# Kernel tuning notes

Hardware: AMD Instinct MI355X
Metric: run time of the kernel (lower is better)

The kernel has to match this reference:

```python
import jax, jax.numpy as jnp
import numpy as np

BETA = 1.0 / np.sqrt(768.0).astype(np.float32)


def setup_inputs() -> dict:
    key = jax.random.key(0)
    k1, k2, k3 = jax.random.split(key, 3)
    x = jax.random.normal(k1, (32, 512, 768), dtype=jnp.float32)
    # torch nn.Linear(dim, n_prototype).weight has shape [n_prototype, dim]
    w_lookup = jax.random.normal(k2, (4096, 768), dtype=jnp.float32) * 0.02
    # torch nn.Linear(n_prototype, dim).weight has shape [dim, n_prototype]
    w_content = jax.random.normal(k3, (768, 4096), dtype=jnp.float32) * 0.02
    return {"x": x, "w_lookup": w_lookup, "w_content": w_content}


def reference(x, w_lookup, w_content):
    # scores: [b, s, n_prototype] = x @ w_lookup^T, scaled by 1/sqrt(dim)
    scores = jnp.einsum("bsd,pd->bsp", x, w_lookup) * jnp.asarray(BETA, x.dtype)
    lookup = jax.nn.softmax(scores, axis=-1)
    # content: [b, s, dim] = lookup @ w_content^T
    content = jnp.einsum("bsp,dp->bsd", lookup, w_content)
    return content  # dropout is identity in eval / p=0.0
```

## Files before the change

### kernel.cpp

```cpp
#include <hip/hip_runtime.h>
#include <hip/hip_bf16.h>


#define NTOK   16384
#define DIM    768
#define NPROT  4096
#define BETA_F 0.03608439182428583f

typedef __bf16 bf16_t;
typedef __bf16 bf16x8 __attribute__((ext_vector_type(8)));
typedef float  floatx4 __attribute__((ext_vector_type(4)));

__device__ __forceinline__ void async_copy16(const bf16_t* g, void* l) {
  __builtin_amdgcn_global_load_lds(
      (__attribute__((address_space(1))) const void*)g,
      (__attribute__((address_space(3))) void*)l, 16, 0, 0);
}

__global__ __launch_bounds__(256) void cvt_all(
    const float* __restrict__ x, const float* __restrict__ wl,
    const float* __restrict__ wc, bf16_t* __restrict__ xb,
    bf16_t* __restrict__ wlb, bf16_t* __restrict__ wcb,
    int nx8, int nw8, int nc8) {
  int i = blockIdx.x * 256 + threadIdx.x;
  const float* in; bf16_t* out; int k;
  if (i < nx8)            { in = x;  out = xb;  k = i; }
  else if (i < nx8 + nw8) { in = wl; out = wlb; k = i - nx8; }
  else if (i < nx8 + nw8 + nc8) { in = wc; out = wcb; k = i - nx8 - nw8; }
  else return;
  const float4* in4 = (const float4*)in;
  float4 a = in4[2 * k], b = in4[2 * k + 1];
  bf16x8 o;
  o[0] = (bf16_t)a.x; o[1] = (bf16_t)a.y; o[2] = (bf16_t)a.z; o[3] = (bf16_t)a.w;
  o[4] = (bf16_t)b.x; o[5] = (bf16_t)b.y; o[6] = (bf16_t)b.z; o[7] = (bf16_t)b.w;
  ((bf16x8*)out)[k] = o;
}

template <int EPI>
__global__ __launch_bounds__(512, 2)
void gemm256(const bf16_t* __restrict__ A, const bf16_t* __restrict__ B,
             void* __restrict__ Cv, float* __restrict__ rowsum,
             const int K, const int N, const int nN) {
  __shared__ char lds[131072];

  const int tid = threadIdx.x;
  const int l   = tid & 63;
  const int w   = tid >> 6;
  const int wr  = w >> 2;
  const int wc  = w & 3;
  const int lr  = l & 15;
  const int lk  = (l >> 4) << 3;

  const int nwg   = gridDim.x;
  const int chunk = nwg >> 3;
  const int wg    = (blockIdx.x & 7) * chunk + (blockIdx.x >> 3);
  const int m0    = (wg / nN) * 256;
  const int n0    = (wg % nN) * 256;

  int aoff[2][2], boff[2][2];
#pragma unroll
  for (int h = 0; h < 2; ++h)
#pragma unroll
    for (int j = 0; j < 2; ++j) {
      const int s     = j * 8 + w;
      const int mfrag = h * 8 + (s >> 1);
      const int ks    = s & 1;
      aoff[h][j] = (m0 + mfrag * 16 + lr) * K + ks * 32 + lk;
      boff[h][j] = (n0 + mfrag * 16 + lr) * K + ks * 32 + lk;
    }

  auto stageA = [&](int slot, int kt, int h) {
#pragma unroll
    for (int j = 0; j < 2; ++j) {
      const int s  = j * 8 + w;
      const int sf = (h * 8 + (s >> 1)) * 2 + (s & 1);
      async_copy16(A + aoff[h][j] + kt * 64, lds + slot * 65536 + sf * 1024);
    }
  };
  auto stageB = [&](int slot, int kt, int h) {
#pragma unroll
    for (int j = 0; j < 2; ++j) {
      const int s  = j * 8 + w;
      const int sf = (h * 8 + (s >> 1)) * 2 + (s & 1);
      async_copy16(B + boff[h][j] + kt * 64,
                   lds + slot * 65536 + 32768 + sf * 1024);
    }
  };

  bf16x8 af[4][2], bg[4][2];
  auto loadA = [&](int slot, int mh) {
#pragma unroll
    for (int q = 0; q < 4; ++q)
#pragma unroll
      for (int ks = 0; ks < 2; ++ks)
        af[q][ks] = *(const bf16x8*)(lds + slot * 65536 +
                        ((mh * 8 + q * 2 + wr) * 2 + ks) * 1024 + l * 16);
  };
  auto loadB = [&](int slot, int nh, int qb) {
#pragma unroll
    for (int q = 0; q < 2; ++q)
#pragma unroll
      for (int ks = 0; ks < 2; ++ks)
        bg[qb + q][ks] = *(const bf16x8*)(lds + slot * 65536 + 32768 +
                        ((nh * 8 + q * 4 + wc) * 2 + ks) * 1024 + l * 16);
  };

  const floatx4 z = {0.f, 0.f, 0.f, 0.f};
  floatx4 acc[8][4];
#pragma unroll
  for (int mt = 0; mt < 8; ++mt)
#pragma unroll
    for (int nt = 0; nt < 4; ++nt) acc[mt][nt] = z;

  auto mma = [&](int mq, int nq) {
    __builtin_amdgcn_s_setprio(1);
#pragma unroll
    for (int q = 0; q < 4; ++q)
#pragma unroll
      for (int r = 0; r < 2; ++r)
#pragma unroll
        for (int ks = 0; ks < 2; ++ks)
          acc[mq * 4 + q][nq * 2 + r] = __builtin_amdgcn_mfma_f32_16x16x32_bf16(
              af[q][ks], bg[nq * 2 + r][ks], acc[mq * 4 + q][nq * 2 + r], 0, 0, 0);
    __builtin_amdgcn_s_setprio(0);
  };

#define BAR()   __builtin_amdgcn_s_barrier()
#define LGKM0() asm volatile("s_waitcnt lgkmcnt(0)" ::: "memory")
#define VM(n)   asm volatile("s_waitcnt vmcnt(" #n ")" ::: "memory")

  const int T = K >> 6;

  stageA(0, 0, 0); stageB(0, 0, 0); stageB(0, 0, 1); stageA(0, 0, 1);
  stageA(1, 1, 0); stageB(1, 1, 0); stageB(1, 1, 1);
  VM(6);
  BAR();

#pragma unroll 1
  for (int t = 0; t < T - 2; t += 2) {
    loadA(0, 0); loadB(0, 0, 0);
    stageA(1, t + 1, 1);
    BAR(); LGKM0(); mma(0, 0); BAR();
    loadB(0, 1, 2);
    stageA(0, t + 2, 0);
    BAR(); LGKM0(); mma(0, 1); BAR();
    loadA(0, 1);
    stageB(0, t + 2, 0);
    BAR(); LGKM0(); mma(1, 1); BAR();
    stageB(0, t + 2, 1);
    BAR(); mma(1, 0); VM(6); BAR();
    loadA(1, 0); loadB(1, 0, 0);
    stageA(0, t + 2, 1);
    BAR(); LGKM0(); mma(0, 0); BAR();
    loadB(1, 1, 2);
    stageA(1, t + 3, 0);
    BAR(); LGKM0(); mma(0, 1); BAR();
    loadA(1, 1);
    stageB(1, t + 3, 0);
    BAR(); LGKM0(); mma(1, 1); BAR();
    stageB(1, t + 3, 1);
    BAR(); mma(1, 0); VM(6); BAR();
  }

  loadA(0, 0); loadB(0, 0, 0);
  stageA(1, T - 1, 1);
  BAR(); LGKM0(); mma(0, 0); BAR();
  loadB(0, 1, 2);
  BAR(); LGKM0(); mma(0, 1); BAR();
  loadA(0, 1);
  BAR(); LGKM0(); mma(1, 1); BAR();
  BAR(); mma(1, 0); VM(0); BAR();
  loadA(1, 0); loadB(1, 0, 0);
  BAR(); LGKM0(); mma(0, 0); BAR();
  loadB(1, 1, 2);
  BAR(); LGKM0(); mma(0, 1); BAR();
  loadA(1, 1);
  BAR(); LGKM0(); mma(1, 1); BAR();
  mma(1, 0);

#undef BAR
#undef LGKM0
#undef VM

  const int hi4 = (l >> 4) << 2;
  if (EPI == 0) {
    bf16_t* P = (bf16_t*)Cv;
#pragma unroll
    for (int mt = 0; mt < 8; ++mt) {
      const int row = m0 + (mt * 2 + wr) * 16 + hi4;
      float rs[4] = {0.f, 0.f, 0.f, 0.f};
#pragma unroll
      for (int nt = 0; nt < 4; ++nt) {
        const int col = n0 + (nt * 4 + wc) * 16 + lr;
#pragma unroll
        for (int i = 0; i < 4; ++i) {
          const float e = __expf(acc[mt][nt][i] * BETA_F);
          P[(row + i) * N + col] = (bf16_t)e;
          rs[i] += e;
        }
      }
#pragma unroll
      for (int i = 0; i < 4; ++i) {
        float s = rs[i];
        s += __shfl_xor(s, 1);
        s += __shfl_xor(s, 2);
        s += __shfl_xor(s, 4);
        s += __shfl_xor(s, 8);
        if (lr == 0) atomicAdd(&rowsum[row + i], s);
      }
    }
  } else {
    float* O = (float*)Cv;
#pragma unroll
    for (int mt = 0; mt < 8; ++mt) {
      const int row = m0 + (mt * 2 + wr) * 16 + hi4;
#pragma unroll
      for (int i = 0; i < 4; ++i) {
        const float inv = 1.0f / rowsum[row + i];
#pragma unroll
        for (int nt = 0; nt < 4; ++nt)
          O[(row + i) * N + n0 + (nt * 4 + wc) * 16 + lr] = acc[mt][nt][i] * inv;
      }
    }
  }
}

__global__ __launch_bounds__(256) void hopfield_fallback(
    const float* __restrict__ x, const float* __restrict__ wl,
    const float* __restrict__ wc, float* __restrict__ out) {
  __shared__ float  xs[8 * 768];
  __shared__ bf16_t ps[8 * 4096];
  __shared__ float  rs[8];
  const int tid = threadIdx.x;
  const int r0  = blockIdx.x * 8;
  if (tid < 8) rs[tid] = 0.f;
  for (int i = tid; i < 8 * 768; i += 256)
    xs[i] = x[(r0 + (i / 768)) * 768 + (i % 768)];
  __syncthreads();

  float lsum[8] = {0, 0, 0, 0, 0, 0, 0, 0};
  for (int p = tid; p < 4096; p += 256) {
    float s[8] = {0, 0, 0, 0, 0, 0, 0, 0};
    for (int d = 0; d < 768; ++d) {
      const float wv = wl[p * 768 + d];
#pragma unroll
      for (int r = 0; r < 8; ++r) s[r] += xs[r * 768 + d] * wv;
    }
#pragma unroll
    for (int r = 0; r < 8; ++r) {
      const float e = __expf(s[r] * BETA_F);
      ps[r * 4096 + p] = (bf16_t)e;
      lsum[r] += e;
    }
  }
#pragma unroll
  for (int r = 0; r < 8; ++r) atomicAdd(&rs[r], lsum[r]);
  __syncthreads();

  for (int d = tid; d < 768; d += 256) {
    float o[8] = {0, 0, 0, 0, 0, 0, 0, 0};
    for (int p = 0; p < 4096; ++p) {
      const float wv = wc[d * 4096 + p];
#pragma unroll
      for (int r = 0; r < 8; ++r) o[r] += (float)ps[r * 4096 + p] * wv;
    }
#pragma unroll
    for (int r = 0; r < 8; ++r) out[(r0 + r) * 768 + d] = o[r] / rs[r];
  }
}

extern "C" void kernel_launch(void* const* d_in, const int* in_sizes, int n_in,
                              void* d_out, int out_size, void* d_ws, size_t ws_size,
                              hipStream_t stream) {
  (void)in_sizes; (void)n_in; (void)out_size;
  const float* x  = (const float*)d_in[0];
  const float* wl = (const float*)d_in[1];
  const float* wc = (const float*)d_in[2];
  float* out = (float*)d_out;

  const size_t xb_e = (size_t)NTOK * DIM;
  const size_t wl_e = (size_t)NPROT * DIM;
  const size_t wc_e = (size_t)DIM * NPROT;
  const size_t P_e  = (size_t)NTOK * NPROT;
  const size_t need = (xb_e + wl_e + wc_e + P_e) * 2 + (size_t)NTOK * 4;

  if (ws_size >= need) {
    char* ws = (char*)d_ws;
    bf16_t* xb  = (bf16_t*)ws;  ws += xb_e * 2;
    bf16_t* wlb = (bf16_t*)ws;  ws += wl_e * 2;
    bf16_t* wcb = (bf16_t*)ws;  ws += wc_e * 2;
    bf16_t* P   = (bf16_t*)ws;  ws += P_e * 2;
    float* rowsum = (float*)ws;

    hipMemsetAsync(rowsum, 0, NTOK * sizeof(float), stream);
    const int nx8 = (int)(xb_e / 8), nw8 = (int)(wl_e / 8), nc8 = (int)(wc_e / 8);
    cvt_all<<<(nx8 + nw8 + nc8 + 255) / 256, 256, 0, stream>>>(
        x, wl, wc, xb, wlb, wcb, nx8, nw8, nc8);
    gemm256<0><<<dim3((NTOK / 256) * (NPROT / 256)), 512, 0, stream>>>(
        xb, wlb, (void*)P, rowsum, DIM, NPROT, NPROT / 256);
    gemm256<1><<<dim3((NTOK / 256) * (DIM / 256)), 512, 0, stream>>>(
        P, wcb, (void*)out, rowsum, NPROT, DIM, DIM / 256);
  } else {
    hopfield_fallback<<<NTOK / 8, 256, 0, stream>>>(x, wl, wc, out);
  }
}
```

Before: 431.3 us.

## Double-buffer LDS fragments in registers to overlap reads with MFMA in GEMM loop

```diff
diff --git a/kernel.cpp b/kernel.cpp
--- a/kernel.cpp
+++ b/kernel.cpp
@@ -87,22 +87,24 @@
     }
   };
 
-  bf16x8 af[4][2], bg[4][2];
-  auto loadA = [&](int slot, int mh) {
-#pragma unroll
-    for (int q = 0; q < 4; ++q)
+  bf16x8 afA[2][2], afB[2][2];
+  bf16x8 bgA[4][2], bgB[4][2];
+
+  auto loadAf = [&](bf16x8 (&dst)[2][2], int slot, int mq) {
+#pragma unroll
+    for (int q = 0; q < 2; ++q)
 #pragma unroll
       for (int ks = 0; ks < 2; ++ks)
-        af[q][ks] = *(const bf16x8*)(lds + slot * 65536 +
-                        ((mh * 8 + q * 2 + wr) * 2 + ks) * 1024 + l * 16);
-  };
-  auto loadB = [&](int slot, int nh, int qb) {
-#pragma unroll
-    for (int q = 0; q < 2; ++q)
+        dst[q][ks] = *(const bf16x8*)(lds + slot * 65536 +
+                        ((4 * mq + 2 * q + wr) * 2 + ks) * 1024 + l * 16);
+  };
+  auto loadBg = [&](bf16x8 (&dst)[4][2], int slot) {
+#pragma unroll
+    for (int nt = 0; nt < 4; ++nt)
 #pragma unroll
       for (int ks = 0; ks < 2; ++ks)
-        bg[qb + q][ks] = *(const bf16x8*)(lds + slot * 65536 + 32768 +
-                        ((nh * 8 + q * 4 + wc) * 2 + ks) * 1024 + l * 16);
+        dst[nt][ks] = *(const bf16x8*)(lds + slot * 65536 + 32768 +
+                        ((nt * 4 + wc) * 2 + ks) * 1024 + l * 16);
   };
 
   const floatx4 z = {0.f, 0.f, 0.f, 0.f};
@@ -112,74 +114,87 @@
 #pragma unroll
     for (int nt = 0; nt < 4; ++nt) acc[mt][nt] = z;
 
-  auto mma = [&](int mq, int nq) {
+  auto mma = [&](const bf16x8 (&af)[2][2], const bf16x8 (&bg)[4][2], int mq) {
     __builtin_amdgcn_s_setprio(1);
 #pragma unroll
-    for (int q = 0; q < 4; ++q)
-#pragma unroll
-      for (int r = 0; r < 2; ++r)
+    for (int q = 0; q < 2; ++q)
+#pragma unroll
+      for (int nt = 0; nt < 4; ++nt)
 #pragma unroll
         for (int ks = 0; ks < 2; ++ks)
-          acc[mq * 4 + q][nq * 2 + r] = __builtin_amdgcn_mfma_f32_16x16x32_bf16(
-              af[q][ks], bg[nq * 2 + r][ks], acc[mq * 4 + q][nq * 2 + r], 0, 0, 0);
+          acc[2 * mq + q][nt] = __builtin_amdgcn_mfma_f32_16x16x32_bf16(
+              af[q][ks], bg[nt][ks], acc[2 * mq + q][nt], 0, 0, 0);
     __builtin_amdgcn_s_setprio(0);
   };
 
-#define BAR()   __builtin_amdgcn_s_barrier()
-#define LGKM0() asm volatile("s_waitcnt lgkmcnt(0)" ::: "memory")
-#define VM(n)   asm volatile("s_waitcnt vmcnt(" #n ")" ::: "memory")
+#define BAR()    do { __builtin_amdgcn_s_barrier(); \
+                      __builtin_amdgcn_sched_barrier(0); } while (0)
+#define VM(n)    asm volatile("s_waitcnt vmcnt(" #n ")" ::: "memory")
 
   const int T = K >> 6;
 
-  stageA(0, 0, 0); stageB(0, 0, 0); stageB(0, 0, 1); stageA(0, 0, 1);
-  stageA(1, 1, 0); stageB(1, 1, 0); stageB(1, 1, 1);
+  stageA(0, 0, 0); stageA(0, 0, 1); stageB(0, 0, 0); stageB(0, 0, 1);
+  stageB(1, 1, 0); stageB(1, 1, 1); stageA(1, 1, 0);
   VM(6);
   BAR();
+  loadAf(afA, 0, 0);
+  loadBg(bgA, 0);
 
 #pragma unroll 1
-  for (int t = 0; t < T - 2; t += 2) {
-    loadA(0, 0); loadB(0, 0, 0);
-    stageA(1, t + 1, 1);
-    BAR(); LGKM0(); mma(0, 0); BAR();
-    loadB(0, 1, 2);
-    stageA(0, t + 2, 0);
-    BAR(); LGKM0(); mma(0, 1); BAR();
-    loadA(0, 1);
-    stageB(0, t + 2, 0);
-    BAR(); LGKM0(); mma(1, 1); BAR();
-    stageB(0, t + 2, 1);
-    BAR(); mma(1, 0); VM(6); BAR();
-    loadA(1, 0); loadB(1, 0, 0);
-    stageA(0, t + 2, 1);
-    BAR(); LGKM0(); mma(0, 0); BAR();
-    loadB(1, 1, 2);
-    stageA(1, t + 3, 0);
-    BAR(); LGKM0(); mma(0, 1); BAR();
-    loadA(1, 1);
-    stageB(1, t + 3, 0);
-    BAR(); LGKM0(); mma(1, 1); BAR();
-    stageB(1, t + 3, 1);
-    BAR(); mma(1, 0); VM(6); BAR();
-  }
-
-  loadA(0, 0); loadB(0, 0, 0);
+  for (int x = 0; x + 3 < T; x += 2) {
+    stageA(1, x + 1, 1);
+    loadAf(afB, 0, 1);
+    mma(afA, bgA, 0); BAR();
+    stageB(0, x + 2, 0);
+    loadAf(afA, 0, 2);
+    mma(afB, bgA, 1); BAR();
+    stageB(0, x + 2, 1);
+    loadAf(afB, 0, 3);
+    mma(afA, bgA, 2);
+    VM(4);
+    BAR();
+    stageA(0, x + 2, 0);
+    loadAf(afA, 1, 0);
+    loadBg(bgB, 1);
+    mma(afB, bgA, 3); BAR();
+    stageA(0, x + 2, 1);
+    loadAf(afB, 1, 1);
+    mma(afA, bgB, 0); BAR();
+    stageB(1, x + 3, 0);
+    loadAf(afA, 1, 2);
+    mma(afB, bgB, 1); BAR();
+    stageB(1, x + 3, 1);
+    loadAf(afB, 1, 3);
+    mma(afA, bgB, 2);
+    VM(4);
+    BAR();
+    stageA(1, x + 3, 0);
+    loadAf(afA, 0, 0);
+    loadBg(bgA, 0);
+    mma(afB, bgB, 3); BAR();
+  }
+
   stageA(1, T - 1, 1);
-  BAR(); LGKM0(); mma(0, 0); BAR();
-  loadB(0, 1, 2);
-  BAR(); LGKM0(); mma(0, 1); BAR();
-  loadA(0, 1);
-  BAR(); LGKM0(); mma(1, 1); BAR();
-  BAR(); mma(1, 0); VM(0); BAR();
-  loadA(1, 0); loadB(1, 0, 0);
-  BAR(); LGKM0(); mma(0, 0); BAR();
-  loadB(1, 1, 2);
-  BAR(); LGKM0(); mma(0, 1); BAR();
-  loadA(1, 1);
-  BAR(); LGKM0(); mma(1, 1); BAR();
-  mma(1, 0);
+  loadAf(afB, 0, 1);
+  mma(afA, bgA, 0); BAR();
+  loadAf(afA, 0, 2);
+  mma(afB, bgA, 1); BAR();
+  loadAf(afB, 0, 3);
+  mma(afA, bgA, 2);
+  VM(0);
+  BAR();
+  loadAf(afA, 1, 0);
+  loadBg(bgB, 1);
+  mma(afB, bgA, 3); BAR();
+  loadAf(afB, 1, 1);
+  mma(afA, bgB, 0); BAR();
+  loadAf(afA, 1, 2);
+  mma(afB, bgB, 1); BAR();
+  loadAf(afB, 1, 3);
+  mma(afA, bgB, 2); BAR();
+  mma(afB, bgB, 3);
 
 #undef BAR
-#undef LGKM0
 #undef VM
 
   const int hi4 = (l >> 4) << 2;
```

Measured after the change: 690.7 us. +60.1%, slower.
